# Kernel tuning notes

Measured on AMD Instinct MI355X. Metric: run time of the kernel, lower is better.

## Reference

```python
import jax, jax.numpy as jnp
import numpy as np

N_NODES = 100000
N_EDGES = 1600000
IN_FEATS = 128
OUT_FEATS = 64


def setup_inputs() -> dict:
    key = jax.random.key(0)
    k1, k2, k3, k4 = jax.random.split(key, 4)
    feat = jax.random.normal(k1, (N_NODES, IN_FEATS), dtype=jnp.float32)
    W = jax.random.normal(k2, (IN_FEATS, OUT_FEATS), dtype=jnp.float32) * (1.0 / np.sqrt(IN_FEATS))
    src = jax.random.randint(k3, (N_EDGES,), 0, N_NODES, dtype=jnp.int64)
    dst = jax.random.randint(k4, (N_EDGES,), 0, N_NODES, dtype=jnp.int64)
    return {"feat": feat, "W": W, "src": src, "dst": dst}


def reference(feat, W, src, dst):
    # Linear projection (bias=False): homogeneous graph -> shared fc
    ft = feat @ W  # [N, out]

    # per-edge dot-product score: e_ij = <ft[src], ft[dst]>
    a = jnp.sum(ft[src] * ft[dst], axis=-1)  # [E]

    # edge softmax segmented by destination node (numerically stable)
    neg_inf = jnp.finfo(a.dtype).min
    m = jax.ops.segment_max(a, dst, num_segments=N_NODES)  # [N]
    m = jnp.where(m == neg_inf, 0.0, m)  # guard zero-in-degree nodes
    e = jnp.exp(a - m[dst])  # [E]
    s = jax.ops.segment_sum(e, dst, num_segments=N_NODES)  # [N]
    s = jnp.where(s == 0.0, 1.0, s)
    sa = e / s[dst]  # [E]

    # weighted scatter-sum aggregation: out[i] = sum_{j in N(i)} sa_ij * ft[j]
    rst = jax.ops.segment_sum(ft[src] * sa[:, None], dst, num_segments=N_NODES)
    return rst
```

## Files before the change

### kernel.cpp

```cpp
#include <hip/hip_runtime.h>
#include <hip/hip_fp16.h>
#include <math.h>

#define N_NODES 100000
#define N_EDGES 1600000
#define IN_F    128
#define OUT_F   64
#define K_BKT     196
#define BKT_SHIFT 9
#define BKT_NODES 512
#define BKT_CAP   10240
#define CHUNK     4096
#define PBLKS     ((N_EDGES + CHUNK - 1) / CHUNK)
#define LTILES    (N_NODES / 16)
#define LBLKS     ((LTILES + 3) / 4)

typedef _Float16 half8 __attribute__((ext_vector_type(8)));
typedef float    f32x4 __attribute__((ext_vector_type(4)));


__global__ __launch_bounds__(256) void partition_linear_kernel(const int* __restrict__ src,
                                                               const int* __restrict__ dst,
                                                               int* __restrict__ bcursor,
                                                               unsigned* __restrict__ staging,
                                                               const float* __restrict__ feat,
                                                               const float* __restrict__ W,
                                                               __half* __restrict__ fth) {
    __shared__ int hist[256], lbase[256], gbase[256], sc[256];
    __shared__ unsigned sval[CHUNK];
    __shared__ int spos[CHUNK];
    int t = threadIdx.x;
    if (blockIdx.x < PBLKS) {
        hist[t] = 0;
        __syncthreads();
        int beg = blockIdx.x * CHUNK;
        int end = min(beg + CHUNK, N_EDGES);
        for (int i = beg + t; i < end; i += 256)
            atomicAdd(&hist[dst[i] >> BKT_SHIFT], 1);
        __syncthreads();
        int v = hist[t];
        sc[t] = v;
        __syncthreads();
        for (int off = 1; off < 256; off <<= 1) {
            int add = (t >= off) ? sc[t - off] : 0;
            __syncthreads();
            sc[t] += add;
            __syncthreads();
        }
        lbase[t] = sc[t] - v;
        if (t < K_BKT && v) gbase[t] = t * BKT_CAP + atomicAdd(&bcursor[t], v);
        hist[t] = 0;
        __syncthreads();
        for (int i = beg + t; i < end; i += 256) {
            int s = src[i], d = dst[i];
            int b = d >> BKT_SHIFT;
            int r = atomicAdd(&hist[b], 1);
            int lp = lbase[b] + r;
            sval[lp] = (unsigned)s | ((unsigned)(d & (BKT_NODES - 1)) << 17);
            spos[lp] = gbase[b] + r;
        }
        __syncthreads();
        int n = end - beg;
        for (int p = t; p < n; p += 256) staging[spos[p]] = sval[p];
        return;
    }
    int gwave = (blockIdx.x - PBLKS) * 4 + (t >> 6);
    if (gwave >= LTILES) return;
    int lane = t & 63;
    int m = lane & 15, kg = lane >> 4;
    int r0 = gwave * 16;

    half8 fb[4][4];
#pragma unroll
    for (int kb = 0; kb < 4; ++kb)
#pragma unroll
        for (int nb = 0; nb < 4; ++nb) {
            const float* wp = W + (size_t)(kb * 32 + kg * 8) * OUT_F + nb * 16 + m;
#pragma unroll
            for (int j = 0; j < 8; ++j)
                fb[kb][nb][j] = (_Float16)wp[j * OUT_F];
        }

    f32x4 acc[4];
#pragma unroll
    for (int nb = 0; nb < 4; ++nb) acc[nb] = (f32x4){0.f, 0.f, 0.f, 0.f};

#pragma unroll
    for (int kb = 0; kb < 4; ++kb) {
        const float4* ap = (const float4*)(feat + (size_t)(r0 + m) * IN_F + kb * 32 + kg * 8);
        float4 a0 = ap[0], a1 = ap[1];
        half8 fa = {(_Float16)a0.x, (_Float16)a0.y, (_Float16)a0.z, (_Float16)a0.w,
                    (_Float16)a1.x, (_Float16)a1.y, (_Float16)a1.z, (_Float16)a1.w};
#pragma unroll
        for (int nb = 0; nb < 4; ++nb)
            acc[nb] = __builtin_amdgcn_mfma_f32_16x16x32_f16(fa, fb[kb][nb], acc[nb], 0, 0, 0);
    }
#pragma unroll
    for (int nb = 0; nb < 4; ++nb)
#pragma unroll
        for (int i = 0; i < 4; ++i)
            fth[(size_t)(r0 + kg * 4 + i) * OUT_F + nb * 16 + m] = __float2half_rn(acc[nb][i]);
}

__global__ __launch_bounds__(256) void place_kernel(const unsigned* __restrict__ staging,
                                                    const int* __restrict__ bcursor,
                                                    int* __restrict__ row_beg,
                                                    int* __restrict__ row_end,
                                                    int* __restrict__ edge_src) {
    __shared__ int cnt[BKT_NODES], sc[256], lcur[BKT_NODES];
    int t = threadIdx.x;
    cnt[t] = 0; cnt[t + 256] = 0;
    __syncthreads();
    int base = blockIdx.x * BKT_CAP;
    int n = bcursor[blockIdx.x];
    for (int i = t; i < n; i += 256)
        atomicAdd(&cnt[staging[base + i] >> 17], 1);
    __syncthreads();
    int v0 = cnt[2 * t], v1 = cnt[2 * t + 1];
    int ts = v0 + v1;
    sc[t] = ts;
    __syncthreads();
    for (int off = 1; off < 256; off <<= 1) {
        int add = (t >= off) ? sc[t - off] : 0;
        __syncthreads();
        sc[t] += add;
        __syncthreads();
    }
    int excl = sc[t] - ts;
    int node0 = blockIdx.x * BKT_NODES;
    int b0 = base + excl, b1 = base + excl + v0;
    lcur[2 * t]     = b0;
    lcur[2 * t + 1] = b1;
    if (node0 + 2 * t < N_NODES)     { row_beg[node0 + 2 * t] = b0;     row_end[node0 + 2 * t] = b0 + v0; }
    if (node0 + 2 * t + 1 < N_NODES) { row_beg[node0 + 2 * t + 1] = b1; row_end[node0 + 2 * t + 1] = b1 + v1; }
    __syncthreads();
    for (int i = base + t; i < base + n; i += 256) {
        unsigned u = staging[i];
        int pos = atomicAdd(&lcur[u >> 17], 1);
        edge_src[pos] = (int)(u & 0x1FFFFu);
    }
}

__global__ __launch_bounds__(256) void fused_node_kernel(const __half* __restrict__ fth,
                                                         const int* __restrict__ row_beg,
                                                         const int* __restrict__ row_end,
                                                         const int* __restrict__ edge_src,
                                                         float* __restrict__ out) {
    const float LOG2E = 1.44269504088896340736f;
    int wave = (blockIdx.x * 256 + threadIdx.x) >> 6;
    int lane = threadIdx.x & 63;
    if (wave >= N_NODES) return;
    int q = lane >> 4, ql = lane & 15;

    int beg = row_beg[wave];
    int end = row_end[wave];

    float2 rd = *(const float2*)(fth + (size_t)wave * OUT_F + 4 * ql);
    __half2 d01 = *(__half2*)&rd.x, d23 = *(__half2*)&rd.y;
    float fd0 = __half2float(d01.x) * LOG2E, fd1 = __half2float(d01.y) * LOG2E;
    float fd2 = __half2float(d23.x) * LOG2E, fd3 = __half2float(d23.y) * LOG2E;

    float m = -1e30f, l = 0.f;
    float a0 = 0.f, a1 = 0.f, a2 = 0.f, a3 = 0.f;

    for (int i = beg; i < end; i += 16) {
        int e0 = i + q, e1 = e0 + 4, e2 = e0 + 8, e3 = e0 + 12;
        bool u0 = e0 < end, u1 = e1 < end, u2 = e2 < end, u3 = e3 < end;
        int s0 = edge_src[u0 ? e0 : beg];
        int s1 = edge_src[u1 ? e1 : beg];
        int s2 = edge_src[u2 ? e2 : beg];
        int s3 = edge_src[u3 ? e3 : beg];
        float2 r0 = *(const float2*)(fth + (size_t)s0 * OUT_F + 4 * ql);
        float2 r1 = *(const float2*)(fth + (size_t)s1 * OUT_F + 4 * ql);
        float2 r2 = *(const float2*)(fth + (size_t)s2 * OUT_F + 4 * ql);
        float2 r3 = *(const float2*)(fth + (size_t)s3 * OUT_F + 4 * ql);
        __half2 A01 = *(__half2*)&r0.x, A23 = *(__half2*)&r0.y;
        __half2 B01 = *(__half2*)&r1.x, B23 = *(__half2*)&r1.y;
        __half2 C01 = *(__half2*)&r2.x, C23 = *(__half2*)&r2.y;
        __half2 D01 = *(__half2*)&r3.x, D23 = *(__half2*)&r3.y;
        float vA0 = __half2float(A01.x), vA1 = __half2float(A01.y);
        float vA2 = __half2float(A23.x), vA3 = __half2float(A23.y);
        float vB0 = __half2float(B01.x), vB1 = __half2float(B01.y);
        float vB2 = __half2float(B23.x), vB3 = __half2float(B23.y);
        float vC0 = __half2float(C01.x), vC1 = __half2float(C01.y);
        float vC2 = __half2float(C23.x), vC3 = __half2float(C23.y);
        float vD0 = __half2float(D01.x), vD1 = __half2float(D01.y);
        float vD2 = __half2float(D23.x), vD3 = __half2float(D23.y);

        float p0 = vA0 * fd0 + vA1 * fd1 + vA2 * fd2 + vA3 * fd3;
        float p1 = vB0 * fd0 + vB1 * fd1 + vB2 * fd2 + vB3 * fd3;
        float p2 = vC0 * fd0 + vC1 * fd1 + vC2 * fd2 + vC3 * fd3;
        float p3 = vD0 * fd0 + vD1 * fd1 + vD2 * fd2 + vD3 * fd3;
#pragma unroll
        for (int dd = 1; dd < 16; dd <<= 1) {
            p0 += __shfl_xor(p0, dd);
            p1 += __shfl_xor(p1, dd);
            p2 += __shfl_xor(p2, dd);
            p3 += __shfl_xor(p3, dd);
        }
        if (!u0) p0 = -1e30f;
        if (!u1) p1 = -1e30f;
        if (!u2) p2 = -1e30f;
        if (!u3) p3 = -1e30f;
        float nm = fmaxf(fmaxf(fmaxf(p0, p1), fmaxf(p2, p3)), m);
        float alpha = exp2f(m - nm);
        float w0 = exp2f(p0 - nm), w1 = exp2f(p1 - nm);
        float w2 = exp2f(p2 - nm), w3 = exp2f(p3 - nm);
        l = l * alpha + ((w0 + w1) + (w2 + w3));
        a0 = a0 * alpha + (w0 * vA0 + w1 * vB0) + (w2 * vC0 + w3 * vD0);
        a1 = a1 * alpha + (w0 * vA1 + w1 * vB1) + (w2 * vC1 + w3 * vD1);
        a2 = a2 * alpha + (w0 * vA2 + w1 * vB2) + (w2 * vC2 + w3 * vD2);
        a3 = a3 * alpha + (w0 * vA3 + w1 * vB3) + (w2 * vC3 + w3 * vD3);
        m = nm;
    }

#pragma unroll
    for (int dd = 16; dd <= 32; dd <<= 1) {
        float m2 = __shfl_xor(m, dd), l2 = __shfl_xor(l, dd);
        float b0 = __shfl_xor(a0, dd), b1 = __shfl_xor(a1, dd);
        float b2 = __shfl_xor(a2, dd), b3 = __shfl_xor(a3, dd);
        float M = fmaxf(m, m2);
        float e1 = exp2f(m - M), e2 = exp2f(m2 - M);
        l = l * e1 + l2 * e2;
        a0 = a0 * e1 + b0 * e2;
        a1 = a1 * e1 + b1 * e2;
        a2 = a2 * e1 + b2 * e2;
        a3 = a3 * e1 + b3 * e2;
        m = M;
    }
    if (q == 0) {
        float inv = (l > 0.f) ? 1.f / l : 0.f;
        *(float4*)(out + (size_t)wave * OUT_F + 4 * ql) =
            make_float4(a0 * inv, a1 * inv, a2 * inv, a3 * inv);
    }
}

extern "C" void kernel_launch(void* const* d_in, const int* in_sizes, int n_in,
                              void* d_out, int out_size, void* d_ws, size_t ws_size,
                              hipStream_t stream) {
    const float* feat = (const float*)d_in[0];
    const float* W    = (const float*)d_in[1];
    const int*   src  = (const int*)d_in[2];
    const int*   dst  = (const int*)d_in[3];
    float* out = (float*)d_out;

    __half*   fth      = (__half*)d_ws;
    unsigned* staging  = (unsigned*)((int*)d_ws + (size_t)N_NODES * OUT_F / 2);
    int*      edge_src = (int*)(staging + (size_t)K_BKT * BKT_CAP);
    int*      bcursor  = edge_src + (size_t)K_BKT * BKT_CAP;
    int*      row_beg  = bcursor + K_BKT;
    int*      row_end  = row_beg + N_NODES;

    hipMemsetAsync(bcursor, 0, K_BKT * sizeof(int), stream);
    partition_linear_kernel<<<PBLKS + LBLKS, 256, 0, stream>>>(src, dst, bcursor, staging,
                                                               feat, W, fth);
    place_kernel<<<K_BKT, 256, 0, stream>>>(staging, bcursor, row_beg, row_end, edge_src);
    fused_node_kernel<<<(N_NODES * 64) / 256, 256, 0, stream>>>(fth, row_beg, row_end, edge_src, out);
}
```

Before: 200.8 us.

## Use MFMA for edge scores and weighted aggregation in fused node kernel

Rewrites the per-node attention kernel to process 16 edges per wave iteration with matrix-core instructions. Dot-product scores come from two 16x16x32 f16 MFMAs, and the weighted sum of neighbor features is done with 16x16x16 MFMAs on an LDS-transposed tile. The shuffle reductions and most scalar FMAs go away. The online-softmax rescale now runs only when the max grows by more than 8 (log2 units), and the weights are rounded to fp16. This adds LDS traffic and wave barriers and loses some precision.

```diff
diff --git a/kernel.cpp b/kernel.cpp
--- a/kernel.cpp
+++ b/kernel.cpp
@@ -16,6 +16,7 @@
 #define LBLKS     ((LTILES + 3) / 4)
 
 typedef _Float16 half8 __attribute__((ext_vector_type(8)));
+typedef _Float16 half4v __attribute__((ext_vector_type(4)));
 typedef float    f32x4 __attribute__((ext_vector_type(4)));
 
 
@@ -147,92 +148,79 @@
                                                          const int* __restrict__ edge_src,
                                                          float* __restrict__ out) {
     const float LOG2E = 1.44269504088896340736f;
+    __shared__ _Float16 slds[4][1280];
     int wave = (blockIdx.x * 256 + threadIdx.x) >> 6;
     int lane = threadIdx.x & 63;
     if (wave >= N_NODES) return;
-    int q = lane >> 4, ql = lane & 15;
+    _Float16* tile = slds[(threadIdx.x >> 6) & 3];
+    int el = lane & 15, kg = lane >> 4;
 
     int beg = row_beg[wave];
     int end = row_end[wave];
 
-    float2 rd = *(const float2*)(fth + (size_t)wave * OUT_F + 4 * ql);
-    __half2 d01 = *(__half2*)&rd.x, d23 = *(__half2*)&rd.y;
-    float fd0 = __half2float(d01.x) * LOG2E, fd1 = __half2float(d01.y) * LOG2E;
-    float fd2 = __half2float(d23.x) * LOG2E, fd3 = __half2float(d23.y) * LOG2E;
+    const _Float16* fh = (const _Float16*)fth;
+    half8 db0 = *(const half8*)(fh + (size_t)wave * OUT_F + kg * 8);
+    half8 db1 = *(const half8*)(fh + (size_t)wave * OUT_F + 32 + kg * 8);
+
+    int widx = ((kg & 1) * 8) + (el & 3) * 16 + (el >> 2) * 80 + (kg >> 1) * 320;
+    int ridx = el + 80 * kg;
 
     float m = -1e30f, l = 0.f;
-    float a0 = 0.f, a1 = 0.f, a2 = 0.f, a3 = 0.f;
+    f32x4 accpv[4];
+#pragma unroll
+    for (int nb = 0; nb < 4; ++nb) accpv[nb] = (f32x4){0.f, 0.f, 0.f, 0.f};
 
     for (int i = beg; i < end; i += 16) {
-        int e0 = i + q, e1 = e0 + 4, e2 = e0 + 8, e3 = e0 + 12;
-        bool u0 = e0 < end, u1 = e1 < end, u2 = e2 < end, u3 = e3 < end;
-        int s0 = edge_src[u0 ? e0 : beg];
-        int s1 = edge_src[u1 ? e1 : beg];
-        int s2 = edge_src[u2 ? e2 : beg];
-        int s3 = edge_src[u3 ? e3 : beg];
-        float2 r0 = *(const float2*)(fth + (size_t)s0 * OUT_F + 4 * ql);
-        float2 r1 = *(const float2*)(fth + (size_t)s1 * OUT_F + 4 * ql);
-        float2 r2 = *(const float2*)(fth + (size_t)s2 * OUT_F + 4 * ql);
-        float2 r3 = *(const float2*)(fth + (size_t)s3 * OUT_F + 4 * ql);
-        __half2 A01 = *(__half2*)&r0.x, A23 = *(__half2*)&r0.y;
-        __half2 B01 = *(__half2*)&r1.x, B23 = *(__half2*)&r1.y;
-        __half2 C01 = *(__half2*)&r2.x, C23 = *(__half2*)&r2.y;
-        __half2 D01 = *(__half2*)&r3.x, D23 = *(__half2*)&r3.y;
-        float vA0 = __half2float(A01.x), vA1 = __half2float(A01.y);
-        float vA2 = __half2float(A23.x), vA3 = __half2float(A23.y);
-        float vB0 = __half2float(B01.x), vB1 = __half2float(B01.y);
-        float vB2 = __half2float(B23.x), vB3 = __half2float(B23.y);
-        float vC0 = __half2float(C01.x), vC1 = __half2float(C01.y);
-        float vC2 = __half2float(C23.x), vC3 = __half2float(C23.y);
-        float vD0 = __half2float(D01.x), vD1 = __half2float(D01.y);
-        float vD2 = __half2float(D23.x), vD3 = __half2float(D23.y);
-
-        float p0 = vA0 * fd0 + vA1 * fd1 + vA2 * fd2 + vA3 * fd3;
-        float p1 = vB0 * fd0 + vB1 * fd1 + vB2 * fd2 + vB3 * fd3;
-        float p2 = vC0 * fd0 + vC1 * fd1 + vC2 * fd2 + vC3 * fd3;
-        float p3 = vD0 * fd0 + vD1 * fd1 + vD2 * fd2 + vD3 * fd3;
-#pragma unroll
-        for (int dd = 1; dd < 16; dd <<= 1) {
-            p0 += __shfl_xor(p0, dd);
-            p1 += __shfl_xor(p1, dd);
-            p2 += __shfl_xor(p2, dd);
-            p3 += __shfl_xor(p3, dd);
-        }
-        if (!u0) p0 = -1e30f;
-        if (!u1) p1 = -1e30f;
-        if (!u2) p2 = -1e30f;
-        if (!u3) p3 = -1e30f;
-        float nm = fmaxf(fmaxf(fmaxf(p0, p1), fmaxf(p2, p3)), m);
-        float alpha = exp2f(m - nm);
-        float w0 = exp2f(p0 - nm), w1 = exp2f(p1 - nm);
-        float w2 = exp2f(p2 - nm), w3 = exp2f(p3 - nm);
-        l = l * alpha + ((w0 + w1) + (w2 + w3));
-        a0 = a0 * alpha + (w0 * vA0 + w1 * vB0) + (w2 * vC0 + w3 * vD0);
-        a1 = a1 * alpha + (w0 * vA1 + w1 * vB1) + (w2 * vC1 + w3 * vD1);
-        a2 = a2 * alpha + (w0 * vA2 + w1 * vB2) + (w2 * vC2 + w3 * vD2);
-        a3 = a3 * alpha + (w0 * vA3 + w1 * vB3) + (w2 * vC3 + w3 * vD3);
-        m = nm;
-    }
-
-#pragma unroll
-    for (int dd = 16; dd <= 32; dd <<= 1) {
-        float m2 = __shfl_xor(m, dd), l2 = __shfl_xor(l, dd);
-        float b0 = __shfl_xor(a0, dd), b1 = __shfl_xor(a1, dd);
-        float b2 = __shfl_xor(a2, dd), b3 = __shfl_xor(a3, dd);
-        float M = fmaxf(m, m2);
-        float e1 = exp2f(m - M), e2 = exp2f(m2 - M);
-        l = l * e1 + l2 * e2;
-        a0 = a0 * e1 + b0 * e2;
-        a1 = a1 * e1 + b1 * e2;
-        a2 = a2 * e1 + b2 * e2;
-        a3 = a3 * e1 + b3 * e2;
-        m = M;
-    }
-    if (q == 0) {
-        float inv = (l > 0.f) ? 1.f / l : 0.f;
-        *(float4*)(out + (size_t)wave * OUT_F + 4 * ql) =
-            make_float4(a0 * inv, a1 * inv, a2 * inv, a3 * inv);
-    }
+        int e = i + el;
+        int ce = (e < end) ? e : beg;
+        int es = edge_src[ce];
+        half8 fa0 = *(const half8*)(fh + (size_t)es * OUT_F + kg * 8);
+        half8 fa1 = *(const half8*)(fh + (size_t)es * OUT_F + 32 + kg * 8);
+        *(half8*)(tile + widx) = fa0;
+        *(half8*)(tile + widx + 640) = fa1;
+
+        f32x4 sc2 = (f32x4){0.f, 0.f, 0.f, 0.f};
+        sc2 = __builtin_amdgcn_mfma_f32_16x16x32_f16(fa0, db0, sc2, 0, 0, 0);
+        sc2 = __builtin_amdgcn_mfma_f32_16x16x32_f16(fa1, db1, sc2, 0, 0, 0);
+
+        int ebase = i + kg * 4;
+        float p0 = (ebase + 0 < end) ? sc2[0] * LOG2E : -1e30f;
+        float p1 = (ebase + 1 < end) ? sc2[1] * LOG2E : -1e30f;
+        float p2 = (ebase + 2 < end) ? sc2[2] * LOG2E : -1e30f;
+        float p3 = (ebase + 3 < end) ? sc2[3] * LOG2E : -1e30f;
+
+        float pm = fmaxf(fmaxf(p0, p1), fmaxf(p2, p3));
+        pm = fmaxf(pm, __shfl_xor(pm, 16));
+        pm = fmaxf(pm, __shfl_xor(pm, 32));
+        if (pm > m + 8.f) {
+            float alpha = exp2f(m - pm);
+            l *= alpha;
+#pragma unroll
+            for (int nb = 0; nb < 4; ++nb) accpv[nb] *= alpha;
+            m = pm;
+        }
+        float w0 = exp2f(p0 - m), w1 = exp2f(p1 - m);
+        float w2 = exp2f(p2 - m), w3 = exp2f(p3 - m);
+        l += (w0 + w1) + (w2 + w3);
+        half4v wh = {(_Float16)w0, (_Float16)w1, (_Float16)w2, (_Float16)w3};
+
+        __builtin_amdgcn_wave_barrier();
+#pragma unroll
+        for (int nb = 0; nb < 4; ++nb) {
+            half4v bf;
+#pragma unroll
+            for (int j = 0; j < 4; ++j) bf[j] = tile[ridx + j * 16 + nb * 320];
+            accpv[nb] = __builtin_amdgcn_mfma_f32_16x16x16f16(wh, bf, accpv[nb], 0, 0, 0);
+        }
+        __builtin_amdgcn_wave_barrier();
+    }
+
+    l += __shfl_xor(l, 16);
+    l += __shfl_xor(l, 32);
+    float inv = (l > 0.f) ? 1.f / l : 0.f;
+    float v = (kg == 0) ? accpv[0][0] : (kg == 1) ? accpv[1][0]
+            : (kg == 2) ? accpv[2][0] : accpv[3][0];
+    out[(size_t)wave * OUT_F + lane] = v * inv;
 }
 
 extern "C" void kernel_launch(void* const* d_in, const int* in_sizes, int n_in,
```

Result: slower. 215.3 us (+7.3%).

## Replace bucketed two-pass edge partition with degree count, scan, atomic scatter CSR

Applied to the files above, without the earlier changes.

Replaces the LDS-based bucket partition plus per-bucket placement with a global degree histogram built by atomics, a block-wise scan that claims segment bases through a global atomic, and an atomic-cursor scatter of source ids into CSR order. This drops the staging buffer and the shared-memory sorting work but adds an extra kernel launch and 1.6M contended global atomics twice. Segments are no longer in ascending node order and edges within a row come out in nondeterministic order, which only changes floating-point summation order. The linear-projection blocks are regrouped to 1024 threads.

```diff
diff --git a/kernel.cpp b/kernel.cpp
--- a/kernel.cpp
+++ b/kernel.cpp
@@ -6,65 +6,30 @@
 #define N_EDGES 1600000
 #define IN_F    128
 #define OUT_F   64
-#define K_BKT     196
-#define BKT_SHIFT 9
-#define BKT_NODES 512
-#define BKT_CAP   10240
 #define CHUNK     4096
-#define PBLKS     ((N_EDGES + CHUNK - 1) / CHUNK)
+#define EBLKS     ((N_EDGES + CHUNK - 1) / CHUNK)
 #define LTILES    (N_NODES / 16)
-#define LBLKS     ((LTILES + 3) / 4)
+#define LIN_BLKS  ((LTILES + 15) / 16)
+#define SC_BLKS   ((N_NODES + 1023) / 1024)
 
 typedef _Float16 half8 __attribute__((ext_vector_type(8)));
 typedef float    f32x4 __attribute__((ext_vector_type(4)));
 
 
-__global__ __launch_bounds__(256) void partition_linear_kernel(const int* __restrict__ src,
-                                                               const int* __restrict__ dst,
-                                                               int* __restrict__ bcursor,
-                                                               unsigned* __restrict__ staging,
-                                                               const float* __restrict__ feat,
-                                                               const float* __restrict__ W,
-                                                               __half* __restrict__ fth) {
-    __shared__ int hist[256], lbase[256], gbase[256], sc[256];
-    __shared__ unsigned sval[CHUNK];
-    __shared__ int spos[CHUNK];
+__global__ __launch_bounds__(1024) void linear_degree_kernel(const int* __restrict__ dst,
+                                                             int* __restrict__ deg,
+                                                             const float* __restrict__ feat,
+                                                             const float* __restrict__ W,
+                                                             __half* __restrict__ fth) {
     int t = threadIdx.x;
-    if (blockIdx.x < PBLKS) {
-        hist[t] = 0;
-        __syncthreads();
-        int beg = blockIdx.x * CHUNK;
+    if (blockIdx.x >= LIN_BLKS) {
+        int beg = (blockIdx.x - LIN_BLKS) * CHUNK;
         int end = min(beg + CHUNK, N_EDGES);
-        for (int i = beg + t; i < end; i += 256)
-            atomicAdd(&hist[dst[i] >> BKT_SHIFT], 1);
-        __syncthreads();
-        int v = hist[t];
-        sc[t] = v;
-        __syncthreads();
-        for (int off = 1; off < 256; off <<= 1) {
-            int add = (t >= off) ? sc[t - off] : 0;
-            __syncthreads();
-            sc[t] += add;
-            __syncthreads();
-        }
-        lbase[t] = sc[t] - v;
-        if (t < K_BKT && v) gbase[t] = t * BKT_CAP + atomicAdd(&bcursor[t], v);
-        hist[t] = 0;
-        __syncthreads();
-        for (int i = beg + t; i < end; i += 256) {
-            int s = src[i], d = dst[i];
-            int b = d >> BKT_SHIFT;
-            int r = atomicAdd(&hist[b], 1);
-            int lp = lbase[b] + r;
-            sval[lp] = (unsigned)s | ((unsigned)(d & (BKT_NODES - 1)) << 17);
-            spos[lp] = gbase[b] + r;
-        }
-        __syncthreads();
-        int n = end - beg;
-        for (int p = t; p < n; p += 256) staging[spos[p]] = sval[p];
+        for (int i = beg + t; i < end; i += 1024)
+            atomicAdd(&deg[dst[i]], 1);
         return;
     }
-    int gwave = (blockIdx.x - PBLKS) * 4 + (t >> 6);
+    int gwave = blockIdx.x * 16 + (t >> 6);
     if (gwave >= LTILES) return;
     int lane = t & 63;
     int m = lane & 15, kg = lane >> 4;
@@ -102,42 +67,44 @@
             fth[(size_t)(r0 + kg * 4 + i) * OUT_F + nb * 16 + m] = __float2half_rn(acc[nb][i]);
 }
 
-__global__ __launch_bounds__(256) void place_kernel(const unsigned* __restrict__ staging,
-                                                    const int* __restrict__ bcursor,
+__global__ __launch_bounds__(1024) void scan_kernel(const int* __restrict__ deg,
+                                                    int* __restrict__ gcur,
                                                     int* __restrict__ row_beg,
                                                     int* __restrict__ row_end,
-                                                    int* __restrict__ edge_src) {
-    __shared__ int cnt[BKT_NODES], sc[256], lcur[BKT_NODES];
+                                                    int* __restrict__ cursor) {
+    __shared__ int s[1024];
+    __shared__ int base;
     int t = threadIdx.x;
-    cnt[t] = 0; cnt[t + 256] = 0;
+    int node = blockIdx.x * 1024 + t;
+    int d = (node < N_NODES) ? deg[node] : 0;
+    s[t] = d;
     __syncthreads();
-    int base = blockIdx.x * BKT_CAP;
-    int n = bcursor[blockIdx.x];
-    for (int i = t; i < n; i += 256)
-        atomicAdd(&cnt[staging[base + i] >> 17], 1);
+    for (int off = 1; off < 1024; off <<= 1) {
+        int add = (t >= off) ? s[t - off] : 0;
+        __syncthreads();
+        s[t] += add;
+        __syncthreads();
+    }
+    if (t == 1023) base = atomicAdd(gcur, s[1023]);
     __syncthreads();
-    int v0 = cnt[2 * t], v1 = cnt[2 * t + 1];
-    int ts = v0 + v1;
-    sc[t] = ts;
-    __syncthreads();
-    for (int off = 1; off < 256; off <<= 1) {
-        int add = (t >= off) ? sc[t - off] : 0;
-        __syncthreads();
-        sc[t] += add;
-        __syncthreads();
-    }
-    int excl = sc[t] - ts;
-    int node0 = blockIdx.x * BKT_NODES;
-    int b0 = base + excl, b1 = base + excl + v0;
-    lcur[2 * t]     = b0;
-    lcur[2 * t + 1] = b1;
-    if (node0 + 2 * t < N_NODES)     { row_beg[node0 + 2 * t] = b0;     row_end[node0 + 2 * t] = b0 + v0; }
-    if (node0 + 2 * t + 1 < N_NODES) { row_beg[node0 + 2 * t + 1] = b1; row_end[node0 + 2 * t + 1] = b1 + v1; }
-    __syncthreads();
-    for (int i = base + t; i < base + n; i += 256) {
-        unsigned u = staging[i];
-        int pos = atomicAdd(&lcur[u >> 17], 1);
-        edge_src[pos] = (int)(u & 0x1FFFFu);
+    if (node < N_NODES) {
+        int b = base + s[t] - d;
+        row_beg[node] = b;
+        row_end[node] = b + d;
+        cursor[node]  = b;
+    }
+}
+
+__global__ __launch_bounds__(1024) void scatter_kernel(const int* __restrict__ src,
+                                                       const int* __restrict__ dst,
+                                                       int* __restrict__ cursor,
+                                                       int* __restrict__ edge_src) {
+    int t = threadIdx.x;
+    int beg = blockIdx.x * CHUNK;
+    int end = min(beg + CHUNK, N_EDGES);
+    for (int i = beg + t; i < end; i += 1024) {
+        int pos = atomicAdd(&cursor[dst[i]], 1);
+        edge_src[pos] = src[i];
     }
 }
 
@@ -244,16 +211,17 @@
     const int*   dst  = (const int*)d_in[3];
     float* out = (float*)d_out;
 
-    __half*   fth      = (__half*)d_ws;
-    unsigned* staging  = (unsigned*)((int*)d_ws + (size_t)N_NODES * OUT_F / 2);
-    int*      edge_src = (int*)(staging + (size_t)K_BKT * BKT_CAP);
-    int*      bcursor  = edge_src + (size_t)K_BKT * BKT_CAP;
-    int*      row_beg  = bcursor + K_BKT;
-    int*      row_end  = row_beg + N_NODES;
-
-    hipMemsetAsync(bcursor, 0, K_BKT * sizeof(int), stream);
-    partition_linear_kernel<<<PBLKS + LBLKS, 256, 0, stream>>>(src, dst, bcursor, staging,
-                                                               feat, W, fth);
-    place_kernel<<<K_BKT, 256, 0, stream>>>(staging, bcursor, row_beg, row_end, edge_src);
+    __half* fth      = (__half*)d_ws;
+    int*    edge_src = (int*)d_ws + (size_t)N_NODES * OUT_F / 2;
+    int*    deg      = edge_src + N_EDGES;
+    int*    gcur     = deg + N_NODES;
+    int*    row_beg  = gcur + 1;
+    int*    row_end  = row_beg + N_NODES;
+    int*    cursor   = row_end + N_NODES;
+
+    (void)hipMemsetAsync(deg, 0, (N_NODES + 1) * sizeof(int), stream);
+    linear_degree_kernel<<<LIN_BLKS + EBLKS, 1024, 0, stream>>>(dst, deg, feat, W, fth);
+    scan_kernel<<<SC_BLKS, 1024, 0, stream>>>(deg, gcur, row_beg, row_end, cursor);
+    scatter_kernel<<<EBLKS, 1024, 0, stream>>>(src, dst, cursor, edge_src);
     fused_node_kernel<<<(N_NODES * 64) / 256, 256, 0, stream>>>(fth, row_beg, row_end, edge_src, out);
 }
```

New measurement: 332.5 us. 1.66x slower.

## Replace global bucket atomics with per-chunk histograms and coalesced staging writes

Applied to the files above, without the earlier changes.

The partition kernel no longer reserves bucket slots through global atomics and scatter-writes edges. It writes each chunk's locally sorted edges contiguously, plus per-chunk per-bucket counts and offsets. The place kernel, now run with 1024 threads per block, scans the counts for its bucket and gathers that bucket's segments from all chunks into shared memory with a binary search per element. This removes the memset, the global atomics and the scattered global writes, at the cost of a strided gather of small segments, two block-wide scans and much higher shared-memory use in place_kernel.

```diff
diff --git a/kernel.cpp b/kernel.cpp
--- a/kernel.cpp
+++ b/kernel.cpp
@@ -21,14 +21,14 @@
 
 __global__ __launch_bounds__(256) void partition_linear_kernel(const int* __restrict__ src,
                                                                const int* __restrict__ dst,
-                                                               int* __restrict__ bcursor,
                                                                unsigned* __restrict__ staging,
+                                                               int* __restrict__ pcnt,
+                                                               int* __restrict__ pbase,
                                                                const float* __restrict__ feat,
                                                                const float* __restrict__ W,
                                                                __half* __restrict__ fth) {
-    __shared__ int hist[256], lbase[256], gbase[256], sc[256];
+    __shared__ int hist[256], lbase[256], sc[256];
     __shared__ unsigned sval[CHUNK];
-    __shared__ int spos[CHUNK];
     int t = threadIdx.x;
     if (blockIdx.x < PBLKS) {
         hist[t] = 0;
@@ -47,21 +47,22 @@
             sc[t] += add;
             __syncthreads();
         }
-        lbase[t] = sc[t] - v;
-        if (t < K_BKT && v) gbase[t] = t * BKT_CAP + atomicAdd(&bcursor[t], v);
+        int lb = sc[t] - v;
+        lbase[t] = lb;
+        pcnt[blockIdx.x * 256 + t]  = v;
+        pbase[blockIdx.x * 256 + t] = lb;
         hist[t] = 0;
         __syncthreads();
         for (int i = beg + t; i < end; i += 256) {
             int s = src[i], d = dst[i];
             int b = d >> BKT_SHIFT;
             int r = atomicAdd(&hist[b], 1);
-            int lp = lbase[b] + r;
-            sval[lp] = (unsigned)s | ((unsigned)(d & (BKT_NODES - 1)) << 17);
-            spos[lp] = gbase[b] + r;
+            sval[lbase[b] + r] = (unsigned)s | ((unsigned)(d & (BKT_NODES - 1)) << 17);
         }
         __syncthreads();
         int n = end - beg;
-        for (int p = t; p < n; p += 256) staging[spos[p]] = sval[p];
+        for (int p = t; p < n; p += 256)
+            staging[(size_t)blockIdx.x * CHUNK + p] = sval[p];
         return;
     }
     int gwave = (blockIdx.x - PBLKS) * 4 + (t >> 6);
@@ -102,40 +103,65 @@
             fth[(size_t)(r0 + kg * 4 + i) * OUT_F + nb * 16 + m] = __float2half_rn(acc[nb][i]);
 }
 
-__global__ __launch_bounds__(256) void place_kernel(const unsigned* __restrict__ staging,
-                                                    const int* __restrict__ bcursor,
-                                                    int* __restrict__ row_beg,
-                                                    int* __restrict__ row_end,
-                                                    int* __restrict__ edge_src) {
-    __shared__ int cnt[BKT_NODES], sc[256], lcur[BKT_NODES];
+__global__ __launch_bounds__(1024) void place_kernel(const unsigned* __restrict__ staging,
+                                                     const int* __restrict__ pcnt,
+                                                     const int* __restrict__ pbase,
+                                                     int* __restrict__ row_beg,
+                                                     int* __restrict__ row_end,
+                                                     int* __restrict__ edge_src) {
+    __shared__ unsigned sbuf[BKT_CAP];
+    __shared__ int exo[PBLKS];
+    __shared__ int pbs[PBLKS];
+    __shared__ int s512[512];
+    __shared__ int cnt[BKT_NODES], lcur[BKT_NODES];
+    __shared__ int ntot;
     int t = threadIdx.x;
-    cnt[t] = 0; cnt[t + 256] = 0;
-    __syncthreads();
-    int base = blockIdx.x * BKT_CAP;
-    int n = bcursor[blockIdx.x];
-    for (int i = t; i < n; i += 256)
-        atomicAdd(&cnt[staging[base + i] >> 17], 1);
-    __syncthreads();
-    int v0 = cnt[2 * t], v1 = cnt[2 * t + 1];
-    int ts = v0 + v1;
-    sc[t] = ts;
-    __syncthreads();
-    for (int off = 1; off < 256; off <<= 1) {
-        int add = (t >= off) ? sc[t - off] : 0;
-        __syncthreads();
-        sc[t] += add;
-        __syncthreads();
-    }
-    int excl = sc[t] - ts;
-    int node0 = blockIdx.x * BKT_NODES;
-    int b0 = base + excl, b1 = base + excl + v0;
-    lcur[2 * t]     = b0;
-    lcur[2 * t + 1] = b1;
-    if (node0 + 2 * t < N_NODES)     { row_beg[node0 + 2 * t] = b0;     row_end[node0 + 2 * t] = b0 + v0; }
-    if (node0 + 2 * t + 1 < N_NODES) { row_beg[node0 + 2 * t + 1] = b1; row_end[node0 + 2 * t + 1] = b1 + v1; }
-    __syncthreads();
-    for (int i = base + t; i < base + n; i += 256) {
-        unsigned u = staging[i];
+    int b = blockIdx.x;
+
+    int d = 0;
+    if (t < PBLKS) { d = pcnt[t * 256 + b]; pbs[t] = pbase[t * 256 + b]; }
+    if (t < 512) { s512[t] = (t < PBLKS) ? d : 0; cnt[t] = 0; }
+    __syncthreads();
+    for (int off = 1; off < 512; off <<= 1) {
+        int add = (t >= off && t < 512) ? s512[t - off] : 0;
+        __syncthreads();
+        if (t < 512) s512[t] += add;
+        __syncthreads();
+    }
+    if (t < PBLKS) exo[t] = s512[t] - d;
+    if (t == PBLKS - 1) ntot = s512[t];
+    __syncthreads();
+    int n = ntot;
+
+    for (int i = t; i < n; i += 1024) {
+        int lo = 0, hi = PBLKS - 1;
+        while (lo < hi) {
+            int mid = (lo + hi + 1) >> 1;
+            if (exo[mid] <= i) lo = mid; else hi = mid - 1;
+        }
+        unsigned u = staging[(size_t)lo * CHUNK + pbs[lo] + (i - exo[lo])];
+        sbuf[i] = u;
+        atomicAdd(&cnt[u >> 17], 1);
+    }
+    __syncthreads();
+    int v = (t < 512) ? cnt[t] : 0;
+    if (t < 512) s512[t] = v;
+    __syncthreads();
+    for (int off = 1; off < 512; off <<= 1) {
+        int add = (t >= off && t < 512) ? s512[t - off] : 0;
+        __syncthreads();
+        if (t < 512) s512[t] += add;
+        __syncthreads();
+    }
+    if (t < 512) {
+        int b0 = b * BKT_CAP + s512[t] - v;
+        lcur[t] = b0;
+        int node = b * BKT_NODES + t;
+        if (node < N_NODES) { row_beg[node] = b0; row_end[node] = b0 + v; }
+    }
+    __syncthreads();
+    for (int i = t; i < n; i += 1024) {
+        unsigned u = sbuf[i];
         int pos = atomicAdd(&lcur[u >> 17], 1);
         edge_src[pos] = (int)(u & 0x1FFFFu);
     }
@@ -246,14 +272,14 @@
 
     __half*   fth      = (__half*)d_ws;
     unsigned* staging  = (unsigned*)((int*)d_ws + (size_t)N_NODES * OUT_F / 2);
-    int*      edge_src = (int*)(staging + (size_t)K_BKT * BKT_CAP);
-    int*      bcursor  = edge_src + (size_t)K_BKT * BKT_CAP;
-    int*      row_beg  = bcursor + K_BKT;
+    int*      edge_src = (int*)(staging + (size_t)PBLKS * CHUNK);
+    int*      pcnt     = edge_src + (size_t)K_BKT * BKT_CAP;
+    int*      pbase    = pcnt + PBLKS * 256;
+    int*      row_beg  = pbase + PBLKS * 256;
     int*      row_end  = row_beg + N_NODES;
 
-    hipMemsetAsync(bcursor, 0, K_BKT * sizeof(int), stream);
-    partition_linear_kernel<<<PBLKS + LBLKS, 256, 0, stream>>>(src, dst, bcursor, staging,
+    partition_linear_kernel<<<PBLKS + LBLKS, 256, 0, stream>>>(src, dst, staging, pcnt, pbase,
                                                                feat, W, fth);
-    place_kernel<<<K_BKT, 256, 0, stream>>>(staging, bcursor, row_beg, row_end, edge_src);
+    place_kernel<<<K_BKT, 1024, 0, stream>>>(staging, pcnt, pbase, row_beg, row_end, edge_src);
     fused_node_kernel<<<(N_NODES * 64) / 256, 256, 0, stream>>>(fth, row_beg, row_end, edge_src, out);
 }
```

Measured after the change: 195.0 us. 2.9% less time.
